# Kernel tuning notes

Hardware: AMD Instinct MI355X
Metric: run time of the kernel (lower is better)

## Reference

```python
import jax, jax.numpy as jnp
import numpy as np

N_WIRES = 4
N_LAYERS = 2
PATCHES = 196  # 14x14 grid of 2x2 patches


def _bexp(a, nd):
    # broadcast angle to rank nd by appending singleton axes
    a = jnp.asarray(a)
    return a.reshape(a.shape + (1,) * (nd - a.ndim))


def _apply_ry(state, wire, angle):
    # state: [B, P, 2,2,2,2]; angle broadcastable to [B, P] or scalar
    st = jnp.moveaxis(state, 2 + wire, -1)
    c = _bexp(jnp.cos(angle * 0.5), st.ndim - 1)
    s = _bexp(jnp.sin(angle * 0.5), st.ndim - 1)
    s0, s1 = st[..., 0], st[..., 1]
    out = jnp.stack([c * s0 - s * s1, s * s0 + c * s1], axis=-1)
    return jnp.moveaxis(out, -1, 2 + wire)


def _apply_cnot(state, control, target):
    st = jnp.moveaxis(state, (2 + control, 2 + target), (-2, -1))
    st = jnp.stack([st[..., 0, :], st[..., 1, ::-1]], axis=-2)
    return jnp.moveaxis(st, (-2, -1), (2 + control, 2 + target))


def _measure_z(state):
    # PauliZ expectation on each wire: sum probs * (+1/-1)
    p = state * state  # real state => |amp|^2
    outs = []
    for w in range(N_WIRES):
        axes = tuple(a for a in range(2, 2 + N_WIRES) if a != 2 + w)
        m = p.sum(axis=axes)  # [B, P, 2]
        outs.append(m[..., 0] - m[..., 1])
    return jnp.stack(outs, axis=-1)  # [B, P, 4]


def _quanv(x, theta):
    B = x.shape[0]
    # extract 2x2 patches: order (r,c),(r,c+1),(r+1,c),(r+1,c+1)
    img = x.reshape(B, 14, 2, 14, 2).transpose(0, 1, 3, 2, 4).reshape(B, PATCHES, 4)
    state = jnp.zeros((B, PATCHES, 16), x.dtype).at[:, :, 0].set(1.0)
    state = state.reshape(B, PATCHES, 2, 2, 2, 2)
    # encoder: RY(x_i) on wire i
    for w in range(N_WIRES):
        state = _apply_ry(state, w, img[:, :, w])
    # variational layers: trainable RY per wire + CNOT ring
    for l in range(N_LAYERS):
        for w in range(N_WIRES):
            state = _apply_ry(state, w, theta[l, w])
        for w in range(N_WIRES):
            state = _apply_cnot(state, w, (w + 1) % N_WIRES)
    return _measure_z(state).reshape(B, PATCHES * N_WIRES)  # [B, 784]


def setup_inputs() -> dict:
    key = jax.random.key(0)
    k = jax.random.split(key, 6)
    B = 4096
    return {
        "x": jax.random.uniform(k[0], (B, 784), jnp.float32),
        "theta": jax.random.normal(k[1], (N_LAYERS, N_WIRES), jnp.float32),
        "W1": jax.random.normal(k[2], (784, 128), jnp.float32) * 0.05,
        "b1": jnp.zeros((128,), jnp.float32),
        "W2": jax.random.normal(k[3], (128, 10), jnp.float32) * 0.05,
        "b2": jnp.zeros((10,), jnp.float32),
    }


def reference(x, theta, W1, b1, W2, b2):
    feats = _quanv(x, theta)                 # [B, 784]
    h = jax.nn.relu(feats @ W1 + b1)          # [B, 128]
    logits = h @ W2 + b2                      # [B, 10]
    return jax.nn.log_softmax(logits, axis=-1)
```

## Files before the change

### kernel.cpp

```cpp
#include <hip/hip_runtime.h>
#include <math.h>

#define PATCHES 196
#define KPAD 800
#define MROWS 16
#define CIRC (MROWS * PATCHES)
#define FRAG_ELEMS (25 * 64 * 8)

typedef short short8 __attribute__((ext_vector_type(8)));
typedef float f32x4 __attribute__((ext_vector_type(4)));

__device__ __forceinline__ unsigned short f2bf(float f) {
  union { float f; unsigned u; } x; x.f = f;
  unsigned r = x.u + 0x7fff + ((x.u >> 16) & 1);
  return (unsigned short)(r >> 16);
}


__global__ __launch_bounds__(256) void w1t_pack_kernel(
    const float* __restrict__ W1, unsigned short* __restrict__ w1p) {
  int idx = blockIdx.x * 256 + threadIdx.x;
  if (idx >= 128 * KPAD) return;
  int n = idx / KPAD;
  int k = idx - n * KPAD;
  float v = (k < 784) ? W1[k * 128 + n] : 0.f;
  int ntile = n >> 4;
  int ki = k >> 5;
  int quad = (k & 31) >> 3;
  int j = k & 7;
  w1p[ntile * FRAG_ELEMS + (ki * 64 + quad * 16 + (n & 15)) * 8 + j] = f2bf(v);
}

__device__ __forceinline__ void apply_ry(float st[16], int bit, float c, float s) {
#pragma unroll
  for (int i = 0; i < 16; ++i) {
    if (!(i & bit)) {
      int j = i | bit;
      float a0 = st[i], a1 = st[j];
      st[i] = c * a0 - s * a1;
      st[j] = s * a0 + c * a1;
    }
  }
}

__device__ __forceinline__ void apply_cnot(float st[16], int cb, int tb) {
#pragma unroll
  for (int i = 0; i < 16; ++i) {
    if ((i & cb) && !(i & tb)) {
      int j = i | tb;
      float t = st[i]; st[i] = st[j]; st[j] = t;
    }
  }
}

__global__ __launch_bounds__(256) void fused_kernel(
    const float* __restrict__ x, const float* __restrict__ theta,
    const unsigned short* __restrict__ w1p, const float* __restrict__ b1,
    const float* __restrict__ W2, const float* __restrict__ b2,
    float* __restrict__ out) {
  __shared__ unsigned short afr[FRAG_ELEMS];
  __shared__ float tc[8], ts[8];
  __shared__ float hs[MROWS * 132];
  __shared__ float ls[MROWS * 10];

  const int tid = threadIdx.x;
  const int row0 = blockIdx.x * MROWS;

  if (tid < 8) {
    float a = 0.5f * theta[tid];
    tc[tid] = __cosf(a);
    ts[tid] = __sinf(a);
  }
  if (tid < 64) {
    int m = tid & 15;
    int qs = tid >> 4;
    int quad = 2 + (qs >> 1);
    int j0 = (qs & 1) * 4;
    ushort4 z; z.x = z.y = z.z = z.w = 0;
    *reinterpret_cast<ushort4*>(afr + (24 * 64 + quad * 16 + m) * 8 + j0) = z;
  }
  __syncthreads();

  for (int c = tid; c < CIRC; c += 256) {
    int bl = c / PATCHES;
    int p = c - bl * PATCHES;
    int pr = p / 14;
    int pc = p - pr * 14;

    const float* xb = x + (size_t)(row0 + bl) * 784 + pr * 56 + pc * 2;
    float v0 = xb[0], v1 = xb[1], v2 = xb[28], v3 = xb[29];

    float st[16];
#pragma unroll
    for (int i = 0; i < 16; ++i) st[i] = 0.f;
    st[0] = 1.f;

    apply_ry(st, 8, __cosf(0.5f * v0), __sinf(0.5f * v0));
    apply_ry(st, 4, __cosf(0.5f * v1), __sinf(0.5f * v1));
    apply_ry(st, 2, __cosf(0.5f * v2), __sinf(0.5f * v2));
    apply_ry(st, 1, __cosf(0.5f * v3), __sinf(0.5f * v3));

#pragma unroll
    for (int l = 0; l < 2; ++l) {
      apply_ry(st, 8, tc[l * 4 + 0], ts[l * 4 + 0]);
      apply_ry(st, 4, tc[l * 4 + 1], ts[l * 4 + 1]);
      apply_ry(st, 2, tc[l * 4 + 2], ts[l * 4 + 2]);
      apply_ry(st, 1, tc[l * 4 + 3], ts[l * 4 + 3]);
      apply_cnot(st, 8, 4);
      apply_cnot(st, 4, 2);
      apply_cnot(st, 2, 1);
      apply_cnot(st, 1, 8);
    }

    float m0 = 0.f, m1 = 0.f, m2 = 0.f, m3 = 0.f;
#pragma unroll
    for (int i = 0; i < 16; ++i) {
      float p2 = st[i] * st[i];
      m0 += (i & 8) ? -p2 : p2;
      m1 += (i & 4) ? -p2 : p2;
      m2 += (i & 2) ? -p2 : p2;
      m3 += (i & 1) ? -p2 : p2;
    }

    int K = p * 4;
    int ki = K >> 5;
    int quad = (K & 31) >> 3;
    int j0 = K & 7;
    ushort4 o;
    o.x = f2bf(m0); o.y = f2bf(m1); o.z = f2bf(m2); o.w = f2bf(m3);
    *reinterpret_cast<ushort4*>(afr + (ki * 64 + quad * 16 + bl) * 8 + j0) = o;
  }
  __syncthreads();

  const int lane = tid & 63;
  const int wave = tid >> 6;
  const int m = lane & 15;
  const int quad = lane >> 4;

  const unsigned short* bp0 = w1p + (size_t)(wave * 2 + 0) * FRAG_ELEMS + lane * 8;
  const unsigned short* bp1 = w1p + (size_t)(wave * 2 + 1) * FRAG_ELEMS + lane * 8;
  const unsigned short* apl = afr + lane * 8;

  f32x4 acc0 = {0.f, 0.f, 0.f, 0.f};
  f32x4 acc1 = {0.f, 0.f, 0.f, 0.f};

#pragma unroll 5
  for (int ki = 0; ki < 25; ++ki) {
    short8 a  = *reinterpret_cast<const short8*>(apl + ki * 512);
    short8 b0 = *reinterpret_cast<const short8*>(bp0 + ki * 512);
    short8 b1f = *reinterpret_cast<const short8*>(bp1 + ki * 512);
    acc0 = __builtin_amdgcn_mfma_f32_16x16x32_bf16(a, b0, acc0, 0, 0, 0);
    acc1 = __builtin_amdgcn_mfma_f32_16x16x32_bf16(a, b1f, acc1, 0, 0, 0);
  }

  {
    const int col0 = (wave * 2 + 0) * 16 + m;
    const int col1 = (wave * 2 + 1) * 16 + m;
    const float bc0 = b1[col0];
    const float bc1 = b1[col1];
#pragma unroll
    for (int r = 0; r < 4; ++r) {
      const int row = quad * 4 + r;
      hs[row * 132 + col0] = fmaxf(acc0[r] + bc0, 0.f);
      hs[row * 132 + col1] = fmaxf(acc1[r] + bc1, 0.f);
    }
  }
  __syncthreads();

  if (tid < MROWS * 10) {
    const int r = tid / 10;
    const int k = tid - r * 10;
    float a = b2[k];
    const float* hr = hs + r * 132;
#pragma unroll 8
    for (int jj = 0; jj < 128; ++jj) a = fmaf(hr[jj], W2[jj * 10 + k], a);
    ls[tid] = a;
  }
  __syncthreads();

  if (tid < MROWS) {
    const int r = tid;
    float mx = ls[r * 10];
#pragma unroll
    for (int k = 1; k < 10; ++k) mx = fmaxf(mx, ls[r * 10 + k]);
    float sum = 0.f;
#pragma unroll
    for (int k = 0; k < 10; ++k) sum += expf(ls[r * 10 + k] - mx);
    const float lse = mx + logf(sum);
    float* orow = out + (size_t)(row0 + r) * 10;
#pragma unroll
    for (int k = 0; k < 10; ++k) orow[k] = ls[r * 10 + k] - lse;
  }
}

extern "C" void kernel_launch(void* const* d_in, const int* in_sizes, int n_in,
                              void* d_out, int out_size, void* d_ws, size_t ws_size,
                              hipStream_t stream) {
  const float* x     = (const float*)d_in[0];
  const float* theta = (const float*)d_in[1];
  const float* W1    = (const float*)d_in[2];
  const float* b1    = (const float*)d_in[3];
  const float* W2    = (const float*)d_in[4];
  const float* b2    = (const float*)d_in[5];
  float* out = (float*)d_out;

  const int B = in_sizes[0] / 784;

  unsigned short* w1p = (unsigned short*)d_ws;

  w1t_pack_kernel<<<(128 * KPAD + 255) / 256, 256, 0, stream>>>(W1, w1p);
  fused_kernel<<<B / MROWS, 256, 0, stream>>>(x, theta, w1p, b1, W2, b2, out);
}
```

Measured before the change: 94.15 us.

## Use 1024-thread blocks with one N-tile per wave and batched MFMA loads

The fused kernel moves from 256 to 1024 threads per block. The quantum-circuit loop now spreads the 3136 circuits over more threads, and the W1 GEMM gives each of 8 waves one 16-column tile instead of two. The MFMA loop loads five A/B fragments before issuing five MFMAs to expose more memory-level parallelism. It also switches log-softmax to fast __expf/__logf. Half the waves sit idle during the GEMM, and the larger blocks may reduce how many blocks fit per CU.

```diff
diff --git a/kernel.cpp b/kernel.cpp
--- a/kernel.cpp
+++ b/kernel.cpp
@@ -15,7 +15,6 @@
   unsigned r = x.u + 0x7fff + ((x.u >> 16) & 1);
   return (unsigned short)(r >> 16);
 }
-
 
 __global__ __launch_bounds__(256) void w1t_pack_kernel(
     const float* __restrict__ W1, unsigned short* __restrict__ w1p) {
@@ -24,11 +23,10 @@
   int n = idx / KPAD;
   int k = idx - n * KPAD;
   float v = (k < 784) ? W1[k * 128 + n] : 0.f;
-  int ntile = n >> 4;
   int ki = k >> 5;
   int quad = (k & 31) >> 3;
   int j = k & 7;
-  w1p[ntile * FRAG_ELEMS + (ki * 64 + quad * 16 + (n & 15)) * 8 + j] = f2bf(v);
+  w1p[(n >> 4) * FRAG_ELEMS + (ki * 64 + quad * 16 + (n & 15)) * 8 + j] = f2bf(v);
 }
 
 __device__ __forceinline__ void apply_ry(float st[16], int bit, float c, float s) {
@@ -53,7 +51,7 @@
   }
 }
 
-__global__ __launch_bounds__(256) void fused_kernel(
+__global__ __launch_bounds__(1024) void fused_kernel(
     const float* __restrict__ x, const float* __restrict__ theta,
     const unsigned short* __restrict__ w1p, const float* __restrict__ b1,
     const float* __restrict__ W2, const float* __restrict__ b2,
@@ -81,7 +79,7 @@
   }
   __syncthreads();
 
-  for (int c = tid; c < CIRC; c += 256) {
+  for (int c = tid; c < CIRC; c += 1024) {
     int bl = c / PATCHES;
     int p = c - bl * PATCHES;
     int pr = p / 14;
@@ -137,33 +135,31 @@
   const int m = lane & 15;
   const int quad = lane >> 4;
 
-  const unsigned short* bp0 = w1p + (size_t)(wave * 2 + 0) * FRAG_ELEMS + lane * 8;
-  const unsigned short* bp1 = w1p + (size_t)(wave * 2 + 1) * FRAG_ELEMS + lane * 8;
-  const unsigned short* apl = afr + lane * 8;
-
-  f32x4 acc0 = {0.f, 0.f, 0.f, 0.f};
-  f32x4 acc1 = {0.f, 0.f, 0.f, 0.f};
-
-#pragma unroll 5
-  for (int ki = 0; ki < 25; ++ki) {
-    short8 a  = *reinterpret_cast<const short8*>(apl + ki * 512);
-    short8 b0 = *reinterpret_cast<const short8*>(bp0 + ki * 512);
-    short8 b1f = *reinterpret_cast<const short8*>(bp1 + ki * 512);
-    acc0 = __builtin_amdgcn_mfma_f32_16x16x32_bf16(a, b0, acc0, 0, 0, 0);
-    acc1 = __builtin_amdgcn_mfma_f32_16x16x32_bf16(a, b1f, acc1, 0, 0, 0);
-  }
-
-  {
-    const int col0 = (wave * 2 + 0) * 16 + m;
-    const int col1 = (wave * 2 + 1) * 16 + m;
-    const float bc0 = b1[col0];
-    const float bc1 = b1[col1];
-#pragma unroll
-    for (int r = 0; r < 4; ++r) {
-      const int row = quad * 4 + r;
-      hs[row * 132 + col0] = fmaxf(acc0[r] + bc0, 0.f);
-      hs[row * 132 + col1] = fmaxf(acc1[r] + bc1, 0.f);
-    }
+  if (wave < 8) {
+    const unsigned short* bp = w1p + (size_t)wave * FRAG_ELEMS + lane * 8;
+    const unsigned short* apl = afr + lane * 8;
+
+    f32x4 acc = {0.f, 0.f, 0.f, 0.f};
+
+#pragma unroll
+    for (int kc = 0; kc < 5; ++kc) {
+      short8 a[5], b[5];
+#pragma unroll
+      for (int u = 0; u < 5; ++u) {
+        const int ki = kc * 5 + u;
+        a[u] = *reinterpret_cast<const short8*>(apl + ki * 512);
+        b[u] = *reinterpret_cast<const short8*>(bp + ki * 512);
+      }
+#pragma unroll
+      for (int u = 0; u < 5; ++u)
+        acc = __builtin_amdgcn_mfma_f32_16x16x32_bf16(a[u], b[u], acc, 0, 0, 0);
+    }
+
+    const int col = wave * 16 + m;
+    const float bc = b1[col];
+#pragma unroll
+    for (int r = 0; r < 4; ++r)
+      hs[(quad * 4 + r) * 132 + col] = fmaxf(acc[r] + bc, 0.f);
   }
   __syncthreads();
 
@@ -185,8 +181,8 @@
     for (int k = 1; k < 10; ++k) mx = fmaxf(mx, ls[r * 10 + k]);
     float sum = 0.f;
 #pragma unroll
-    for (int k = 0; k < 10; ++k) sum += expf(ls[r * 10 + k] - mx);
-    const float lse = mx + logf(sum);
+    for (int k = 0; k < 10; ++k) sum += __expf(ls[r * 10 + k] - mx);
+    const float lse = mx + __logf(sum);
     float* orow = out + (size_t)(row0 + r) * 10;
 #pragma unroll
     for (int k = 0; k < 10; ++k) orow[k] = ls[r * 10 + k] - lse;
@@ -209,5 +205,5 @@
   unsigned short* w1p = (unsigned short*)d_ws;
 
   w1t_pack_kernel<<<(128 * KPAD + 255) / 256, 256, 0, stream>>>(W1, w1p);
-  fused_kernel<<<B / MROWS, 256, 0, stream>>>(x, theta, w1p, b1, W2, b2, out);
-}
+  fused_kernel<<<B / MROWS, 1024, 0, stream>>>(x, theta, w1p, b1, W2, b2, out);
+}
```

Result: faster. 89.49 us (-5.0%).
